# Optimization experiments

Measured on AMD Instinct MI355X. Metric: run time of the kernel, lower is better.

## Reference

```python
import jax, jax.numpy as jnp
import numpy as np

B, S, TEXT_DIM, VISION_DIM, HIDDEN, HEADS = 4, 2048, 768, 768, 512, 8
HEAD_DIM = HIDDEN // HEADS


def setup_inputs() -> dict:
    key = jax.random.key(0)
    ks = jax.random.split(key, 9)
    s_in = 1.0 / np.sqrt(TEXT_DIM)
    s_h = 1.0 / np.sqrt(HIDDEN)
    return {
        "text_embeds": jax.random.normal(ks[0], (B, S, TEXT_DIM), dtype=jnp.float32),
        "Wq": jax.random.uniform(ks[1], (TEXT_DIM, HIDDEN), jnp.float32, -s_in, s_in),
        "bq": jax.random.uniform(ks[2], (HIDDEN,), jnp.float32, -s_in, s_in),
        "Wk": jax.random.uniform(ks[3], (TEXT_DIM, HIDDEN), jnp.float32, -s_in, s_in),
        "bk": jax.random.uniform(ks[4], (HIDDEN,), jnp.float32, -s_in, s_in),
        "Wv": jax.random.uniform(ks[5], (TEXT_DIM, HIDDEN), jnp.float32, -s_in, s_in),
        "bv": jax.random.uniform(ks[6], (HIDDEN,), jnp.float32, -s_in, s_in),
        "Wo": jax.random.uniform(ks[7], (HIDDEN, VISION_DIM), jnp.float32, -s_h, s_h),
        "bo": jax.random.uniform(ks[8], (VISION_DIM,), jnp.float32, -s_h, s_h),
    }


def reference(text_embeds, Wq, bq, Wk, bk, Wv, bv, Wo, bo):
    b, s, _ = text_embeds.shape
    # QKV projections -> [b, heads, s, head_dim]
    def proj(W, bias):
        y = jnp.einsum("bsd,dh->bsh", text_embeds, W) + bias
        return y.reshape(b, s, HEADS, HEAD_DIM).transpose(0, 2, 1, 3)
    q, k, v = proj(Wq, bq), proj(Wk, bk), proj(Wv, bv)
    scores = jnp.einsum("bhqd,bhkd->bhqk", q, k) / np.sqrt(HEAD_DIM).astype(np.float32)
    weights = jax.nn.softmax(scores, axis=-1)
    attended = jnp.einsum("bhqk,bhkd->bhqd", weights, v)
    attended = attended.transpose(0, 2, 1, 3).reshape(b, s, HIDDEN)
    out = jnp.einsum("bsh,hv->bsv", attended, Wo) + bo
    return jnp.squeeze(out, axis=1) if out.shape[1] == 1 else out
```

## Files before the change

### kernel.cpp

```cpp
#include <hip/hip_runtime.h>
#include <hip/hip_bf16.h>

#define BATCH 4
#define SEQ 2048
#define TDIM 768
#define VDIM 768
#define HID 512
#define NHEADS 8
#define HDIM 64
#define MROWS (BATCH * SEQ)
#define NQKV (3 * HID)

typedef unsigned short ushort_t;
typedef __attribute__((ext_vector_type(8))) short short8;
typedef __attribute__((ext_vector_type(4))) short short4v;
typedef __attribute__((ext_vector_type(4))) float floatx4;
typedef __attribute__((ext_vector_type(16))) float floatx16;

#define QSCALE 0.18033688011112042f

__device__ __forceinline__ ushort_t bf16_rne(float f) {
    unsigned int u = __float_as_uint(f);
    u = (u + 0x7fffu + ((u >> 16) & 1u)) >> 16;
    return (ushort_t)u;
}

__device__ __forceinline__ void async16(const ushort_t* g, ushort_t* l) {
    __builtin_amdgcn_global_load_lds(
        (const __attribute__((address_space(1))) unsigned int*)g,
        (__attribute__((address_space(3))) unsigned int*)l, 16, 0, 0);
}

__global__ __launch_bounds__(256) void conv_x(const float* __restrict__ X,
                                              ushort_t* __restrict__ Xb)
{
    const int i = (blockIdx.x * 256 + threadIdx.x) * 4;
    const floatx4 v = *(const floatx4*)(X + i);
    short4v o;
#pragma unroll
    for (int j = 0; j < 4; ++j) o[j] = (short)bf16_rne(v[j]);
    *(short4v*)(Xb + i) = o;
}

__global__ __launch_bounds__(256) void transp_w(
    const float* __restrict__ Wq, const float* __restrict__ Wk,
    const float* __restrict__ Wv, const float* __restrict__ Wo,
    ushort_t* __restrict__ Wqkvt, ushort_t* __restrict__ Wot)
{
    __shared__ float tile[32][33];
    const int z = blockIdx.z;
    const float* src;
    ushort_t* dst;
    int R, C;
    if (z < 3) {
        src = (z == 0) ? Wq : (z == 1) ? Wk : Wv;
        dst = Wqkvt + (size_t)z * HID * TDIM;
        R = TDIM; C = HID;
    } else {
        src = Wo; dst = Wot; R = HID; C = VDIM;
    }
    const int tx = threadIdx.x & 31, ty = threadIdx.x >> 5;
    const int c0 = blockIdx.x * 32, r0 = blockIdx.y * 32;
    if (c0 >= C || r0 >= R) return;
#pragma unroll
    for (int i = 0; i < 4; ++i)
        tile[ty + i * 8][tx] = src[(size_t)(r0 + ty + i * 8) * C + c0 + tx];
    __syncthreads();
#pragma unroll
    for (int i = 0; i < 4; ++i)
        dst[(size_t)(c0 + ty + i * 8) * R + r0 + tx] = bf16_rne(tile[tx][ty + i * 8]);
}

template<int KD, bool SWAPPED>
__device__ __forceinline__ void gemm128(
    const ushort_t* __restrict__ A, const ushort_t* __restrict__ Bt,
    int m0, int n0, ushort_t* As, ushort_t* Bs, floatx4 (&acc)[4][4])
{
    const int tid  = threadIdx.x;
    const int lane = tid & 63;
    const int w    = tid >> 6;
    const int l15  = lane & 15;
    const int quad = lane >> 4;
    const int wrow = w >> 1;
    const int wcol = w & 1;

    const int srow = lane >> 3;
    const int scol = ((lane & 7) ^ srow) * 8;

    const ushort_t* ga = A  + (size_t)(m0 + w * 32 + srow) * KD + scol;
    const ushort_t* gb = Bt + (size_t)(n0 + w * 32 + srow) * KD + scol;
    ushort_t* la = As + (w * 32) * 64;
    ushort_t* lb = Bs + (w * 32) * 64;

    for (int kt = 0; kt < KD; kt += 64) {
#pragma unroll
        for (int i = 0; i < 4; ++i) {
            async16(ga + (size_t)(i * 8) * KD + kt, la + i * 8 * 64);
            async16(gb + (size_t)(i * 8) * KD + kt, lb + i * 8 * 64);
        }
        __syncthreads();
#pragma unroll
        for (int half = 0; half < 2; ++half) {
            const int kk = ((half * 4 + quad) ^ (l15 & 7)) * 8;
            short8 af[4], bf[4];
#pragma unroll
            for (int t = 0; t < 4; ++t) {
                af[t] = *(const short8*)&As[(wrow * 64 + t * 16 + l15) * 64 + kk];
                bf[t] = *(const short8*)&Bs[(wcol * 64 + t * 16 + l15) * 64 + kk];
            }
#pragma unroll
            for (int mi = 0; mi < 4; ++mi)
#pragma unroll
                for (int ni = 0; ni < 4; ++ni) {
                    if (SWAPPED)
                        acc[mi][ni] = __builtin_amdgcn_mfma_f32_16x16x32_bf16(
                            bf[ni], af[mi], acc[mi][ni], 0, 0, 0);
                    else
                        acc[mi][ni] = __builtin_amdgcn_mfma_f32_16x16x32_bf16(
                            af[mi], bf[ni], acc[mi][ni], 0, 0, 0);
                }
        }
        __syncthreads();
    }
}

__global__ __launch_bounds__(256) void qkv_gemm_mfma(
    const ushort_t* __restrict__ Xb, const ushort_t* __restrict__ Wt,
    const float* __restrict__ bq, const float* __restrict__ bk,
    const float* __restrict__ bv,
    ushort_t* __restrict__ Q, ushort_t* __restrict__ K, ushort_t* __restrict__ V)
{
    __shared__ __align__(16) ushort_t As[128 * 64];
    __shared__ __align__(16) ushort_t Bs[128 * 64];

    const int bx = blockIdx.x;
    const int m0 = blockIdx.y * 128;
    const int n0 = bx * 128;
    const int which = bx >> 2;
    const bool isV = (which == 2);

    floatx4 acc[4][4];
#pragma unroll
    for (int i = 0; i < 4; ++i)
#pragma unroll
        for (int j = 0; j < 4; ++j) acc[i][j] = (floatx4)0.0f;

    if (isV) gemm128<TDIM, false>(Xb, Wt, m0, n0, As, Bs, acc);
    else     gemm128<TDIM, true >(Xb, Wt, m0, n0, As, Bs, acc);

    const int lane = threadIdx.x & 63;
    const int w    = threadIdx.x >> 6;
    const int l15  = lane & 15;
    const int quad = lane >> 4;
    const int wrow = w >> 1;
    const int wcol = w & 1;

    if (!isV) {
        const float* bias = (which == 0) ? bq : bk;
        const float scale = (which == 0) ? QSCALE : 1.0f;
        ushort_t* Out = (which == 0) ? Q : K;
#pragma unroll
        for (int mi = 0; mi < 4; ++mi) {
            const int m = m0 + wrow * 64 + mi * 16 + l15;
            const int b = m >> 11;
            const int s = m & 2047;
#pragma unroll
            for (int ni = 0; ni < 4; ++ni) {
                const int c = (n0 - which * HID) + wcol * 64 + ni * 16 + quad * 4;
                const int h = c >> 6;
                const int d0 = c & 63;
                const floatx4 b4 = *(const floatx4*)(bias + c);
                short4v pk;
#pragma unroll
                for (int r = 0; r < 4; ++r)
                    pk[r] = (short)bf16_rne((acc[mi][ni][r] + b4[r]) * scale);
                *(short4v*)&Out[((size_t)(b * NHEADS + h) * SEQ + s) * HDIM + d0] = pk;
            }
        }
    } else {
#pragma unroll
        for (int ni = 0; ni < 4; ++ni) {
            const int c = (n0 - 2 * HID) + wcol * 64 + ni * 16 + l15;
            const int h = c >> 6;
            const int d = c & 63;
            const float b1 = bv[c];
#pragma unroll
            for (int mi = 0; mi < 4; ++mi) {
                const int mb = m0 + wrow * 64 + mi * 16 + quad * 4;
                const int b = mb >> 11;
                const int s0 = mb & 2047;
                short4v pk;
#pragma unroll
                for (int r = 0; r < 4; ++r)
                    pk[r] = (short)bf16_rne(acc[mi][ni][r] + b1);
                *(short4v*)&V[((size_t)(b * NHEADS + h) * HDIM + d) * SEQ + s0] = pk;
            }
        }
    }
}

__global__ __launch_bounds__(512) void flash_attn_mfma(
    const ushort_t* __restrict__ Q, const ushort_t* __restrict__ K,
    const ushort_t* __restrict__ Vt, ushort_t* __restrict__ Att)
{
    __shared__ __align__(16) ushort_t Ks[2][64 * 64];
    __shared__ __align__(16) ushort_t Vs[2][64 * 64];

    const int tid  = threadIdx.x;
    const int lane = tid & 63;
    const int w    = tid >> 6;
    const int l31  = lane & 31;
    const int hi   = lane >> 5;
    const int r7   = l31 & 7;
    const int a3   = l31 >> 3;

    const int bh = blockIdx.y;
    const int b  = bh >> 3;
    const int h  = bh & 7;
    const int q0 = blockIdx.x * 256;

    const ushort_t* Qb = Q  + (size_t)bh * SEQ * HDIM;
    const ushort_t* Kb = K  + (size_t)bh * SEQ * HDIM;
    const ushort_t* Vb = Vt + (size_t)bh * HDIM * SEQ;

    short8 qf[4];
    {
        const ushort_t* qrow = Qb + (size_t)(q0 + w * 32 + l31) * HDIM + hi * 8;
#pragma unroll
        for (int d = 0; d < 4; ++d) qf[d] = *(const short8*)(qrow + d * 16);
    }

    floatx16 of0 = (floatx16)0.0f;
    floatx16 of1 = (floatx16)0.0f;
    float l_run = 0.f;

    const floatx16 z16 = (floatx16)0.0f;

    const int srow = lane >> 3;
    const int scol = (((lane & 7) ^ srow) ^ w) * 8;
    const ushort_t* gk = Kb + (size_t)(w * 8 + srow) * HDIM + scol;
    const ushort_t* gv = Vb + (size_t)(w * 8 + srow) * SEQ + scol;
    ushort_t* lk0 = &Ks[0][w * 8 * 64];
    ushort_t* lk1 = &Ks[1][w * 8 * 64];
    ushort_t* lv0 = &Vs[0][w * 8 * 64];
    ushort_t* lv1 = &Vs[1][w * 8 * 64];

    auto tile = [&](const ushort_t* Kt, const ushort_t* Vt_) {
        floatx16 sacc0 = z16, sacc1 = z16;
        __builtin_amdgcn_s_setprio(1);
#pragma unroll
        for (int d = 0; d < 4; ++d) {
            const int sl = ((2 * d + hi) ^ r7 ^ a3) * 8;
            const short8 kf0 = *(const short8*)&Kt[l31 * 64 + sl];
            const short8 kf1 = *(const short8*)&Kt[(32 + l31) * 64 + (sl ^ 32)];
            sacc0 = __builtin_amdgcn_mfma_f32_32x32x16_bf16(kf0, qf[d], sacc0, 0, 0, 0);
            sacc1 = __builtin_amdgcn_mfma_f32_32x32x16_bf16(kf1, qf[d], sacc1, 0, 0, 0);
        }
        __builtin_amdgcn_s_setprio(0);

        unsigned ua[8], ub[8];
        float rs = 0.f;
#pragma unroll
        for (int g = 0; g < 4; ++g) {
            const float p0 = __builtin_amdgcn_exp2f(sacc0[g * 4 + 0]);
            const float p1 = __builtin_amdgcn_exp2f(sacc0[g * 4 + 1]);
            const float p2 = __builtin_amdgcn_exp2f(sacc0[g * 4 + 2]);
            const float p3 = __builtin_amdgcn_exp2f(sacc0[g * 4 + 3]);
            rs += (p0 + p1) + (p2 + p3);
            asm("v_cvt_pk_bf16_f32 %0, %1, %2" : "=v"(ua[2 * g])     : "v"(p0), "v"(p1));
            asm("v_cvt_pk_bf16_f32 %0, %1, %2" : "=v"(ua[2 * g + 1]) : "v"(p2), "v"(p3));
        }
#pragma unroll
        for (int g = 0; g < 4; ++g) {
            const float p0 = __builtin_amdgcn_exp2f(sacc1[g * 4 + 0]);
            const float p1 = __builtin_amdgcn_exp2f(sacc1[g * 4 + 1]);
            const float p2 = __builtin_amdgcn_exp2f(sacc1[g * 4 + 2]);
            const float p3 = __builtin_amdgcn_exp2f(sacc1[g * 4 + 3]);
            rs += (p0 + p1) + (p2 + p3);
            asm("v_cvt_pk_bf16_f32 %0, %1, %2" : "=v"(ub[2 * g])     : "v"(p0), "v"(p1));
            asm("v_cvt_pk_bf16_f32 %0, %1, %2" : "=v"(ub[2 * g + 1]) : "v"(p2), "v"(p3));
        }
        l_run += rs;

        short8 pfr[4];
#pragma unroll
        for (int t = 0; t < 2; ++t) {
            unsigned x0 = ua[4 * t + 0], y0 = ua[4 * t + 2];
            asm("v_permlane32_swap_b32 %0, %1" : "+v"(x0), "+v"(y0));
            unsigned x1 = ua[4 * t + 1], y1 = ua[4 * t + 3];
            asm("v_permlane32_swap_b32 %0, %1" : "+v"(x1), "+v"(y1));
            union { unsigned u[4]; short8 s8; } P;
            P.u[0] = x0; P.u[1] = x1; P.u[2] = y0; P.u[3] = y1;
            pfr[t] = P.s8;
        }
#pragma unroll
        for (int t = 0; t < 2; ++t) {
            unsigned x0 = ub[4 * t + 0], y0 = ub[4 * t + 2];
            asm("v_permlane32_swap_b32 %0, %1" : "+v"(x0), "+v"(y0));
            unsigned x1 = ub[4 * t + 1], y1 = ub[4 * t + 3];
            asm("v_permlane32_swap_b32 %0, %1" : "+v"(x1), "+v"(y1));
            union { unsigned u[4]; short8 s8; } P;
            P.u[0] = x0; P.u[1] = x1; P.u[2] = y0; P.u[3] = y1;
            pfr[2 + t] = P.s8;
        }

        __builtin_amdgcn_s_setprio(1);
#pragma unroll
        for (int ks = 0; ks < 4; ++ks) {
            const int sl = ((2 * ks + hi) ^ r7 ^ a3) * 8;
            const short8 vf0 = *(const short8*)&Vt_[l31 * 64 + sl];
            const short8 vf1 = *(const short8*)&Vt_[(32 + l31) * 64 + (sl ^ 32)];
            of0 = __builtin_amdgcn_mfma_f32_32x32x16_bf16(vf0, pfr[ks], of0, 0, 0, 0);
            of1 = __builtin_amdgcn_mfma_f32_32x32x16_bf16(vf1, pfr[ks], of1, 0, 0, 0);
        }
        __builtin_amdgcn_s_setprio(0);
    };

    async16(gk, lk0);
    async16(gv, lv0);

    for (int kt = 0; kt < SEQ; kt += 128) {
        __syncthreads();
        async16(gk + (size_t)(kt + 64) * HDIM, lk1);
        async16(gv + (kt + 64), lv1);
        tile(Ks[0], Vs[0]);

        __syncthreads();
        if (kt + 128 < SEQ) {
            async16(gk + (size_t)(kt + 128) * HDIM, lk0);
            async16(gv + (kt + 128), lv0);
        }
        tile(Ks[1], Vs[1]);
    }

    l_run += __shfl_xor(l_run, 32);
    const float inv = 1.f / l_run;

    const int s = q0 + w * 32 + l31;
    ushort_t* arow = Att + ((size_t)(b * SEQ + s)) * HID + h * HDIM;
#pragma unroll
    for (int rq = 0; rq < 4; ++rq) {
        short4v pk0, pk1;
#pragma unroll
        for (int j = 0; j < 4; ++j) {
            pk0[j] = (short)bf16_rne(of0[rq * 4 + j] * inv);
            pk1[j] = (short)bf16_rne(of1[rq * 4 + j] * inv);
        }
        *(short4v*)&arow[rq * 8 + hi * 4]      = pk0;
        *(short4v*)&arow[32 + rq * 8 + hi * 4] = pk1;
    }
}

__global__ __launch_bounds__(256) void out_gemm_mfma(
    const ushort_t* __restrict__ Attb, const ushort_t* __restrict__ Wot,
    const float* __restrict__ bo, float* __restrict__ Y)
{
    __shared__ __align__(16) ushort_t As[128 * 64];
    __shared__ __align__(16) ushort_t Bs[128 * 64];

    const int m0 = blockIdx.y * 128;
    const int n0 = blockIdx.x * 128;

    floatx4 acc[4][4];
#pragma unroll
    for (int i = 0; i < 4; ++i)
#pragma unroll
        for (int j = 0; j < 4; ++j) acc[i][j] = (floatx4)0.0f;

    gemm128<HID, true>(Attb, Wot, m0, n0, As, Bs, acc);

    const int lane = threadIdx.x & 63;
    const int w    = threadIdx.x >> 6;
    const int l15  = lane & 15;
    const int quad = lane >> 4;
    const int wrow = w >> 1;
    const int wcol = w & 1;

#pragma unroll
    for (int mi = 0; mi < 4; ++mi) {
        const int m = m0 + wrow * 64 + mi * 16 + l15;
#pragma unroll
        for (int ni = 0; ni < 4; ++ni) {
            const int nb = n0 + wcol * 64 + ni * 16 + quad * 4;
            const floatx4 b4 = *(const floatx4*)(bo + nb);
            floatx4 o;
#pragma unroll
            for (int r = 0; r < 4; ++r) o[r] = acc[mi][ni][r] + b4[r];
            *(floatx4*)&Y[(size_t)m * VDIM + nb] = o;
        }
    }
}

extern "C" void kernel_launch(void* const* d_in, const int* in_sizes, int n_in,
                              void* d_out, int out_size, void* d_ws, size_t ws_size,
                              hipStream_t stream)
{
    const float* text = (const float*)d_in[0];
    const float* Wq = (const float*)d_in[1];
    const float* bq = (const float*)d_in[2];
    const float* Wk = (const float*)d_in[3];
    const float* bk = (const float*)d_in[4];
    const float* Wv = (const float*)d_in[5];
    const float* bv = (const float*)d_in[6];
    const float* Wo = (const float*)d_in[7];
    const float* bo = (const float*)d_in[8];
    float* out = (float*)d_out;

    ushort_t* Xb    = (ushort_t*)d_ws;
    ushort_t* Wqkvt = Xb + (size_t)MROWS * TDIM;
    ushort_t* Wot   = Wqkvt + (size_t)NQKV * TDIM;
    ushort_t* Qw    = Wot + (size_t)VDIM * HID;
    ushort_t* Kw    = Qw + (size_t)MROWS * HID;
    ushort_t* Vtw   = Kw + (size_t)MROWS * HID;
    ushort_t* Attb  = Vtw + (size_t)MROWS * HID;

    conv_x<<<dim3(MROWS * TDIM / 1024), 256, 0, stream>>>(text, Xb);
    transp_w<<<dim3(24, 24, 4), 256, 0, stream>>>(Wq, Wk, Wv, Wo, Wqkvt, Wot);
    qkv_gemm_mfma<<<dim3(12, 64), 256, 0, stream>>>(Xb, Wqkvt, bq, bk, bv, Qw, Kw, Vtw);
    flash_attn_mfma<<<dim3(8, 32), 512, 0, stream>>>(Qw, Kw, Vtw, Attb);
    out_gemm_mfma<<<dim3(6, 64), 256, 0, stream>>>(Attb, Wot, bo, out);
}
```

Baseline: 190.2 us.

## Split KV range across two wave groups in flash attention and reduce via LDS

Each attention block now handles 128 queries instead of 256. Its 8 waves form two groups that each process half of the key/value sequence with their own double-buffered LDS tiles. The partial outputs and row sums are summed through LDS, and the first group writes the normalized result. The grid doubles so more blocks are available across CUs, at the cost of more LDS per block, doubled K/V loads per query block, and an extra reduction phase.

```diff
diff --git a/kernel.cpp b/kernel.cpp
--- a/kernel.cpp
+++ b/kernel.cpp
@@ -203,12 +203,13 @@
     const ushort_t* __restrict__ Q, const ushort_t* __restrict__ K,
     const ushort_t* __restrict__ Vt, ushort_t* __restrict__ Att)
 {
-    __shared__ __align__(16) ushort_t Ks[2][64 * 64];
-    __shared__ __align__(16) ushort_t Vs[2][64 * 64];
+    __shared__ __align__(16) ushort_t KVs[2][2][2][64 * 64];
 
     const int tid  = threadIdx.x;
     const int lane = tid & 63;
     const int w    = tid >> 6;
+    const int g    = w >> 2;
+    const int wl   = w & 3;
     const int l31  = lane & 31;
     const int hi   = lane >> 5;
     const int r7   = l31 & 7;
@@ -217,7 +218,7 @@
     const int bh = blockIdx.y;
     const int b  = bh >> 3;
     const int h  = bh & 7;
-    const int q0 = blockIdx.x * 256;
+    const int q0 = blockIdx.x * 128;
 
     const ushort_t* Qb = Q  + (size_t)bh * SEQ * HDIM;
     const ushort_t* Kb = K  + (size_t)bh * SEQ * HDIM;
@@ -225,7 +226,7 @@
 
     short8 qf[4];
     {
-        const ushort_t* qrow = Qb + (size_t)(q0 + w * 32 + l31) * HDIM + hi * 8;
+        const ushort_t* qrow = Qb + (size_t)(q0 + wl * 32 + l31) * HDIM + hi * 8;
 #pragma unroll
         for (int d = 0; d < 4; ++d) qf[d] = *(const short8*)(qrow + d * 16);
     }
@@ -236,14 +237,22 @@
 
     const floatx16 z16 = (floatx16)0.0f;
 
-    const int srow = lane >> 3;
-    const int scol = (((lane & 7) ^ srow) ^ w) * 8;
-    const ushort_t* gk = Kb + (size_t)(w * 8 + srow) * HDIM + scol;
-    const ushort_t* gv = Vb + (size_t)(w * 8 + srow) * SEQ + scol;
-    ushort_t* lk0 = &Ks[0][w * 8 * 64];
-    ushort_t* lk1 = &Ks[1][w * 8 * 64];
-    ushort_t* lv0 = &Vs[0][w * 8 * 64];
-    ushort_t* lv1 = &Vs[1][w * 8 * 64];
+    const int srow  = lane >> 3;
+    const int scol0 = (((lane & 7) ^ srow) ^ (wl * 2 + 0)) * 8;
+    const int scol1 = (((lane & 7) ^ srow) ^ (wl * 2 + 1)) * 8;
+    const int ktg   = g * 1024;
+
+    const ushort_t* gk0 = Kb + (size_t)(wl * 16 + srow) * HDIM + scol0;
+    const ushort_t* gk1 = Kb + (size_t)(wl * 16 + 8 + srow) * HDIM + scol1;
+    const ushort_t* gv0 = Vb + (size_t)(wl * 16 + srow) * SEQ + scol0;
+    const ushort_t* gv1 = Vb + (size_t)(wl * 16 + 8 + srow) * SEQ + scol1;
+
+    auto stage = [&](int buf, int kt) {
+        async16(gk0 + (size_t)kt * HDIM, &KVs[g][buf][0][(wl * 16) * 64]);
+        async16(gk1 + (size_t)kt * HDIM, &KVs[g][buf][0][(wl * 16 + 8) * 64]);
+        async16(gv0 + kt,                &KVs[g][buf][1][(wl * 16) * 64]);
+        async16(gv1 + kt,                &KVs[g][buf][1][(wl * 16 + 8) * 64]);
+    };
 
     auto tile = [&](const ushort_t* Kt, const ushort_t* Vt_) {
         floatx16 sacc0 = z16, sacc1 = z16;
@@ -261,24 +270,24 @@
         unsigned ua[8], ub[8];
         float rs = 0.f;
 #pragma unroll
-        for (int g = 0; g < 4; ++g) {
-            const float p0 = __builtin_amdgcn_exp2f(sacc0[g * 4 + 0]);
-            const float p1 = __builtin_amdgcn_exp2f(sacc0[g * 4 + 1]);
-            const float p2 = __builtin_amdgcn_exp2f(sacc0[g * 4 + 2]);
-            const float p3 = __builtin_amdgcn_exp2f(sacc0[g * 4 + 3]);
+        for (int gq = 0; gq < 4; ++gq) {
+            const float p0 = __builtin_amdgcn_exp2f(sacc0[gq * 4 + 0]);
+            const float p1 = __builtin_amdgcn_exp2f(sacc0[gq * 4 + 1]);
+            const float p2 = __builtin_amdgcn_exp2f(sacc0[gq * 4 + 2]);
+            const float p3 = __builtin_amdgcn_exp2f(sacc0[gq * 4 + 3]);
             rs += (p0 + p1) + (p2 + p3);
-            asm("v_cvt_pk_bf16_f32 %0, %1, %2" : "=v"(ua[2 * g])     : "v"(p0), "v"(p1));
-            asm("v_cvt_pk_bf16_f32 %0, %1, %2" : "=v"(ua[2 * g + 1]) : "v"(p2), "v"(p3));
-        }
-#pragma unroll
-        for (int g = 0; g < 4; ++g) {
-            const float p0 = __builtin_amdgcn_exp2f(sacc1[g * 4 + 0]);
-            const float p1 = __builtin_amdgcn_exp2f(sacc1[g * 4 + 1]);
-            const float p2 = __builtin_amdgcn_exp2f(sacc1[g * 4 + 2]);
-            const float p3 = __builtin_amdgcn_exp2f(sacc1[g * 4 + 3]);
+            asm("v_cvt_pk_bf16_f32 %0, %1, %2" : "=v"(ua[2 * gq])     : "v"(p0), "v"(p1));
+            asm("v_cvt_pk_bf16_f32 %0, %1, %2" : "=v"(ua[2 * gq + 1]) : "v"(p2), "v"(p3));
+        }
+#pragma unroll
+        for (int gq = 0; gq < 4; ++gq) {
+            const float p0 = __builtin_amdgcn_exp2f(sacc1[gq * 4 + 0]);
+            const float p1 = __builtin_amdgcn_exp2f(sacc1[gq * 4 + 1]);
+            const float p2 = __builtin_amdgcn_exp2f(sacc1[gq * 4 + 2]);
+            const float p3 = __builtin_amdgcn_exp2f(sacc1[gq * 4 + 3]);
             rs += (p0 + p1) + (p2 + p3);
-            asm("v_cvt_pk_bf16_f32 %0, %1, %2" : "=v"(ub[2 * g])     : "v"(p0), "v"(p1));
-            asm("v_cvt_pk_bf16_f32 %0, %1, %2" : "=v"(ub[2 * g + 1]) : "v"(p2), "v"(p3));
+            asm("v_cvt_pk_bf16_f32 %0, %1, %2" : "=v"(ub[2 * gq])     : "v"(p0), "v"(p1));
+            asm("v_cvt_pk_bf16_f32 %0, %1, %2" : "=v"(ub[2 * gq + 1]) : "v"(p2), "v"(p3));
         }
         l_run += rs;
 
@@ -316,38 +325,53 @@
         __builtin_amdgcn_s_setprio(0);
     };
 
-    async16(gk, lk0);
-    async16(gv, lv0);
-
-    for (int kt = 0; kt < SEQ; kt += 128) {
+    stage(0, ktg);
+
+    for (int kt = ktg; kt < ktg + 1024; kt += 128) {
         __syncthreads();
-        async16(gk + (size_t)(kt + 64) * HDIM, lk1);
-        async16(gv + (kt + 64), lv1);
-        tile(Ks[0], Vs[0]);
+        stage(1, kt + 64);
+        tile(KVs[g][0][0], KVs[g][0][1]);
 
         __syncthreads();
-        if (kt + 128 < SEQ) {
-            async16(gk + (size_t)(kt + 128) * HDIM, lk0);
-            async16(gv + (kt + 128), lv0);
-        }
-        tile(Ks[1], Vs[1]);
-    }
-
-    l_run += __shfl_xor(l_run, 32);
-    const float inv = 1.f / l_run;
-
-    const int s = q0 + w * 32 + l31;
-    ushort_t* arow = Att + ((size_t)(b * SEQ + s)) * HID + h * HDIM;
-#pragma unroll
-    for (int rq = 0; rq < 4; ++rq) {
-        short4v pk0, pk1;
-#pragma unroll
-        for (int j = 0; j < 4; ++j) {
-            pk0[j] = (short)bf16_rne(of0[rq * 4 + j] * inv);
-            pk1[j] = (short)bf16_rne(of1[rq * 4 + j] * inv);
-        }
-        *(short4v*)&arow[rq * 8 + hi * 4]      = pk0;
-        *(short4v*)&arow[32 + rq * 8 + hi * 4] = pk1;
+        if (kt + 128 < ktg + 1024) stage(0, kt + 128);
+        tile(KVs[g][1][0], KVs[g][1][1]);
+    }
+
+    __syncthreads();
+    float* Cf = (float*)KVs;
+    float* Lf = Cf + 32 * 256;
+    if (g == 1) {
+#pragma unroll
+        for (int j = 0; j < 16; ++j) {
+            Cf[j * 256 + wl * 64 + lane]        = of0[j];
+            Cf[(16 + j) * 256 + wl * 64 + lane] = of1[j];
+        }
+        Lf[wl * 64 + lane] = l_run;
+    }
+    __syncthreads();
+    if (g == 0) {
+#pragma unroll
+        for (int j = 0; j < 16; ++j) {
+            of0[j] += Cf[j * 256 + wl * 64 + lane];
+            of1[j] += Cf[(16 + j) * 256 + wl * 64 + lane];
+        }
+        l_run += Lf[wl * 64 + lane];
+        l_run += __shfl_xor(l_run, 32);
+        const float inv = 1.f / l_run;
+
+        const int s = q0 + wl * 32 + l31;
+        ushort_t* arow = Att + ((size_t)(b * SEQ + s)) * HID + h * HDIM;
+#pragma unroll
+        for (int rq = 0; rq < 4; ++rq) {
+            short4v pk0, pk1;
+#pragma unroll
+            for (int j = 0; j < 4; ++j) {
+                pk0[j] = (short)bf16_rne(of0[rq * 4 + j] * inv);
+                pk1[j] = (short)bf16_rne(of1[rq * 4 + j] * inv);
+            }
+            *(short4v*)&arow[rq * 8 + hi * 4]      = pk0;
+            *(short4v*)&arow[32 + rq * 8 + hi * 4] = pk1;
+        }
     }
 }
 
@@ -417,6 +441,6 @@
     conv_x<<<dim3(MROWS * TDIM / 1024), 256, 0, stream>>>(text, Xb);
     transp_w<<<dim3(24, 24, 4), 256, 0, stream>>>(Wq, Wk, Wv, Wo, Wqkvt, Wot);
     qkv_gemm_mfma<<<dim3(12, 64), 256, 0, stream>>>(Xb, Wqkvt, bq, bk, bv, Qw, Kw, Vtw);
-    flash_attn_mfma<<<dim3(8, 32), 512, 0, stream>>>(Qw, Kw, Vtw, Attb);
+    flash_attn_mfma<<<dim3(16, 32), 512, 0, stream>>>(Qw, Kw, Vtw, Attb);
     out_gemm_mfma<<<dim3(6, 64), 256, 0, stream>>>(Attb, Wot, bo, out);
 }
```

After: 192.0 us. About the same (+1.0%).
